# Kernel tuning notes

Measured on AMD Instinct MI355X. Metric: run time of the kernel, lower is better.

The kernel has to match this reference:

```python
import math
import jax, jax.numpy as jnp
import numpy as np

D_MODEL = 1024
L_MAX = 4096
BATCH = 2
FILTER_ORDER = 64
EMB_DIM = 3


def _make_z(L, emb_dim=EMB_DIM):
    # PositionalEmbedding: [time, real bands, imag bands] -> [1, L, emb_dim]
    t = jnp.linspace(0.0, 1.0, L)[None, :, None]
    bands = (emb_dim - 1) // 2
    t_res = jnp.linspace(0.0, L - 1.0, L)[None, :, None]
    w = 2.0 * math.pi * t_res / L
    f = jnp.linspace(1e-4, float(bands - 1), bands)[None, None]
    ph = f * w  # z = exp(-1j*ph) -> real=cos(ph), imag=-sin(ph)
    return jnp.concatenate([t, jnp.cos(ph), -jnp.sin(ph)], axis=-1).astype(jnp.float32)


def setup_inputs() -> dict:
    key = jax.random.key(0)
    ks = jax.random.split(key, 16)
    d = D_MODEL
    iw = 3 * d  # inner_width = d_model * (order + 1), order=2

    def rn(k, shape, scale):
        return (jax.random.normal(k, shape) * scale).astype(jnp.float32)

    return {
        'u': rn(ks[0], (BATCH, L_MAX, d), 1.0),
        'w_in': rn(ks[1], (iw, d), d ** -0.5),
        'b_in': rn(ks[2], (iw,), 0.01),
        'sf_w': rn(ks[3], (iw, 1, 3), 3 ** -0.5),
        'sf_b': rn(ks[4], (iw,), 0.01),
        'z': _make_z(L_MAX),
        'w0': rn(ks[5], (FILTER_ORDER, EMB_DIM), EMB_DIM ** -0.5),
        'b0': rn(ks[6], (FILTER_ORDER,), 0.01),
        'freq': jnp.ones((1, FILTER_ORDER), dtype=jnp.float32),  # Sin(w=1)
        'w1': rn(ks[7], (FILTER_ORDER, FILTER_ORDER), FILTER_ORDER ** -0.5),
        'b1': rn(ks[8], (FILTER_ORDER,), 0.01),
        'w2': rn(ks[9], (FILTER_ORDER, FILTER_ORDER), FILTER_ORDER ** -0.5),
        'b2': rn(ks[10], (FILTER_ORDER,), 0.01),
        'wf': rn(ks[11], (d, FILTER_ORDER), FILTER_ORDER ** -0.5),
        'D': rn(ks[12], (d,), 1.0),
        'w_out': rn(ks[13], (d, d), d ** -0.5),
        'b_out': rn(ks[14], (d,), 0.01),
    }


def _dwconv(x, w, b):
    # depthwise Conv1d(kernel=3, padding=2, groups=C); x: [B, C, L] -> [B, C, L+2]
    y = jax.lax.conv_general_dilated(
        x, w, window_strides=(1,), padding=[(2, 2)],
        feature_group_count=x.shape[1],
        dimension_numbers=('NCH', 'OIH', 'NCH'))
    return y + b[None, :, None]


def _fftconv(v, k, D):
    # circular conv via zero-padded FFT; torch's k_f/fft_size with norm='forward'
    # irfft cancels to the standard (norm='backward') inverse.
    L = v.shape[-1]
    n = 2 * L
    y = jnp.fft.irfft(jnp.fft.rfft(v, n=n) * jnp.fft.rfft(k, n=n), n=n)[..., :L]
    return y + v * D[:, None]


def reference(u, w_in, b_in, sf_w, sf_b, z, w0, b0, freq, w1, b1, w2, b2, wf, D, w_out, b_out):
    b, l, d = u.shape
    L = min(l, L_MAX)

    # input projection + short depthwise filter
    up = jnp.einsum('bld,ed->ble', u, w_in) + b_in  # [b, l, 3d]
    up = up.transpose(0, 2, 1)                       # [b, 3d, l]
    uc = _dwconv(up, sf_w, sf_b)[..., :L]            # [b, 3d, L]
    x0, x1, v = jnp.split(uc, 3, axis=1)             # each [b, d, L]

    # implicit filter MLP with shared Sin activation
    h = jnp.sin(freq * (z @ w0.T + b0))              # [1, L, 64]
    h = jnp.sin(freq * (h @ w1.T + b1))
    h = jnp.sin(freq * (h @ w2.T + b2))
    h = h @ wf.T                                     # [1, L, d]

    # exponential modulation (buffers: t, deltas)
    t = jnp.linspace(0.0, 1.0, L)[None, :, None]
    max_decay = math.log(0.01) / 0.3
    min_decay = math.log(0.01) / 1.5
    deltas = jnp.linspace(min_decay, max_decay, d)[None, None]
    h = h * jnp.exp(-t * jnp.abs(deltas))            # [1, L, d]
    k = h[0].T                                       # [d, L]

    # hyena recurrence (order=2 -> one gated fft conv)
    v = _fftconv(v * x1, k, D)
    y = (v * x0).transpose(0, 2, 1)                  # [b, L, d]
    return jnp.einsum('bld,ed->ble', y, w_out) + b_out
```

## Files before the change

kernel.cpp:

```cpp
#include <hip/hip_runtime.h>
#include <math.h>

#define DM   1024
#define LL   4096
#define NB   2
#define E3   3072
#define FPI  3.14159265358979323846f

typedef __bf16 bf16x8 __attribute__((ext_vector_type(8)));
typedef float  f32x4  __attribute__((ext_vector_type(4)));
typedef _Float16 f16x2 __attribute__((ext_vector_type(2)));

__device__ __forceinline__ unsigned short f2bf(float x) {
    unsigned u = __float_as_uint(x);
    u += 0x7fffu + ((u >> 16) & 1u);
    return (unsigned short)(u >> 16);
}
__device__ __forceinline__ void gload16(void* lds, const void* g) {
    typedef const __attribute__((address_space(1))) unsigned int* gp_t;
    typedef __attribute__((address_space(3))) unsigned int* lp_t;
    __builtin_amdgcn_global_load_lds((gp_t)g, (lp_t)lds, 16, 0, 0);
}

__global__ __launch_bounds__(256) void k_cvt_bf16(
    const float* __restrict__ in, ushort* __restrict__ out, int n4)
{
    int idx = blockIdx.x * 256 + threadIdx.x;
    int stride = gridDim.x * 256;
    for (int i = idx; i < n4; i += stride) {
        float4 v = reinterpret_cast<const float4*>(in)[i];
        ushort4 o;
        o.x = f2bf(v.x); o.y = f2bf(v.y); o.z = f2bf(v.z); o.w = f2bf(v.w);
        *reinterpret_cast<ushort4*>(out + 4 * i) = o;
    }
}

__global__ __launch_bounds__(512, 2) void k_gemm256(
    const ushort* __restrict__ A, const ushort* __restrict__ B,
    const float* __restrict__ bias, float* __restrict__ C,
    int Ntiles, int ldc)
{
    __shared__ __align__(16) char ldsm[131072];
    const int tid  = threadIdx.x;
    const int lane = tid & 63;
    const int w    = tid >> 6;
    const int wr   = w >> 2, wc = w & 3;

    const int cpx = gridDim.x >> 3;
    int swz = (blockIdx.x & 7) * cpx + (blockIdx.x >> 3);
    const int m0 = (swz / Ntiles) << 8;
    const int n0 = (swz % Ntiles) << 8;

    const int r0 = tid >> 2;
    const int swzc = ((tid & 3) ^ ((r0 >> 1) & 3)) << 4;
    const char* Asrc = (const char*)A + ((size_t)(m0 + r0) << 11) + swzc;
    const char* Bsrc = (const char*)B + ((size_t)(n0 + r0) << 11) + swzc;
    char* Ld = ldsm + tid * 16;

    const int lm = lane & 15, lk = lane >> 4;
    const int rA = wr * 128 + lm;
    const int rB = wc * 64 + lm;
    const int aBase = rA * 64 + ((lk ^ ((rA >> 1) & 3)) << 4);
    const int bBase = 32768 + rB * 64 + ((lk ^ ((rB >> 1) & 3)) << 4);

#define STG_A(ks, nb, t1) do { \
    gload16(Ld + (nb) + (ks)*16384,        Asrc + (t1)*128 + (ks)*64); \
    gload16(Ld + (nb) + (ks)*16384 + 8192, Asrc + (t1)*128 + (ks)*64 + 262144); } while(0)
#define STG_B(ks, nb, t1) do { \
    gload16(Ld + (nb) + 32768 + (ks)*16384,        Bsrc + (t1)*128 + (ks)*64); \
    gload16(Ld + (nb) + 32768 + (ks)*16384 + 8192, Bsrc + (t1)*128 + (ks)*64 + 262144); } while(0)
#define LDA(buf, ks, m) (*(const bf16x8*)(ldsm + (buf) + (ks)*16384 + aBase + (m)*1024))
#define LDB(buf, ks, n) (*(const bf16x8*)(ldsm + (buf) + (ks)*16384 + bBase + (n)*1024))
#define VMCNT4() asm volatile("s_waitcnt vmcnt(4)" ::: "memory")
#define VMCNT0() asm volatile("s_waitcnt vmcnt(0)" ::: "memory")
#define BAR() __builtin_amdgcn_s_barrier()

    f32x4 acc[8][4];
#pragma unroll
    for (int i = 0; i < 8; ++i)
#pragma unroll
        for (int j = 0; j < 4; ++j)
#pragma unroll
            for (int r = 0; r < 4; ++r) acc[i][j][r] = 0.f;

    STG_A(0, 0, 0); STG_B(0, 0, 0); STG_A(1, 0, 0); STG_B(1, 0, 0);
    VMCNT4();
    BAR();

    bf16x8 af[4], bq[4];
#pragma unroll 1
    for (int t = 0; t < 15; ++t) {
        const int buf = (t & 1) << 16;
        const int nb  = ((t + 1) & 1) << 16;
        const int t1  = t + 1;
#pragma unroll
        for (int n = 0; n < 4; ++n) bq[n] = LDB(buf, 0, n);
#pragma unroll
        for (int m = 0; m < 4; ++m) af[m] = LDA(buf, 0, m);
        STG_A(0, nb, t1);
        BAR();
        __builtin_amdgcn_s_setprio(1);
#pragma unroll
        for (int m = 0; m < 4; ++m)
#pragma unroll
            for (int n = 0; n < 4; ++n)
                acc[m][n] = __builtin_amdgcn_mfma_f32_16x16x32_bf16(af[m], bq[n], acc[m][n], 0, 0, 0);
        __builtin_amdgcn_s_setprio(0);
        BAR();
#pragma unroll
        for (int m = 0; m < 4; ++m) af[m] = LDA(buf, 0, 4 + m);
        STG_B(0, nb, t1);
        VMCNT4();
        BAR();
        __builtin_amdgcn_s_setprio(1);
#pragma unroll
        for (int m = 0; m < 4; ++m)
#pragma unroll
            for (int n = 0; n < 4; ++n)
                acc[4 + m][n] = __builtin_amdgcn_mfma_f32_16x16x32_bf16(af[m], bq[n], acc[4 + m][n], 0, 0, 0);
        __builtin_amdgcn_s_setprio(0);
        BAR();
#pragma unroll
        for (int n = 0; n < 4; ++n) bq[n] = LDB(buf, 1, n);
#pragma unroll
        for (int m = 0; m < 4; ++m) af[m] = LDA(buf, 1, m);
        STG_A(1, nb, t1);
        BAR();
        __builtin_amdgcn_s_setprio(1);
#pragma unroll
        for (int m = 0; m < 4; ++m)
#pragma unroll
            for (int n = 0; n < 4; ++n)
                acc[m][n] = __builtin_amdgcn_mfma_f32_16x16x32_bf16(af[m], bq[n], acc[m][n], 0, 0, 0);
        __builtin_amdgcn_s_setprio(0);
        BAR();
#pragma unroll
        for (int m = 0; m < 4; ++m) af[m] = LDA(buf, 1, 4 + m);
        STG_B(1, nb, t1);
        VMCNT4();
        BAR();
        __builtin_amdgcn_s_setprio(1);
#pragma unroll
        for (int m = 0; m < 4; ++m)
#pragma unroll
            for (int n = 0; n < 4; ++n)
                acc[4 + m][n] = __builtin_amdgcn_mfma_f32_16x16x32_bf16(af[m], bq[n], acc[4 + m][n], 0, 0, 0);
        __builtin_amdgcn_s_setprio(0);
        BAR();
    }
    {
        const int buf = 1 << 16;
#pragma unroll
        for (int n = 0; n < 4; ++n) bq[n] = LDB(buf, 0, n);
#pragma unroll
        for (int m = 0; m < 4; ++m) af[m] = LDA(buf, 0, m);
        BAR();
#pragma unroll
        for (int m = 0; m < 4; ++m)
#pragma unroll
            for (int n = 0; n < 4; ++n)
                acc[m][n] = __builtin_amdgcn_mfma_f32_16x16x32_bf16(af[m], bq[n], acc[m][n], 0, 0, 0);
        BAR();
#pragma unroll
        for (int m = 0; m < 4; ++m) af[m] = LDA(buf, 0, 4 + m);
        VMCNT0();
        BAR();
#pragma unroll
        for (int m = 0; m < 4; ++m)
#pragma unroll
            for (int n = 0; n < 4; ++n)
                acc[4 + m][n] = __builtin_amdgcn_mfma_f32_16x16x32_bf16(af[m], bq[n], acc[4 + m][n], 0, 0, 0);
        BAR();
#pragma unroll
        for (int n = 0; n < 4; ++n) bq[n] = LDB(buf, 1, n);
#pragma unroll
        for (int m = 0; m < 4; ++m) af[m] = LDA(buf, 1, m);
        BAR();
#pragma unroll
        for (int m = 0; m < 4; ++m)
#pragma unroll
            for (int n = 0; n < 4; ++n)
                acc[m][n] = __builtin_amdgcn_mfma_f32_16x16x32_bf16(af[m], bq[n], acc[m][n], 0, 0, 0);
        BAR();
#pragma unroll
        for (int m = 0; m < 4; ++m) af[m] = LDA(buf, 1, 4 + m);
        BAR();
#pragma unroll
        for (int m = 0; m < 4; ++m)
#pragma unroll
            for (int n = 0; n < 4; ++n)
                acc[4 + m][n] = __builtin_amdgcn_mfma_f32_16x16x32_bf16(af[m], bq[n], acc[4 + m][n], 0, 0, 0);
    }
    const int er = lk << 2, ec = lm;
#pragma unroll
    for (int m = 0; m < 8; ++m) {
        int row = m0 + wr * 128 + m * 16 + er;
#pragma unroll
        for (int n = 0; n < 4; ++n) {
            int col = n0 + wc * 64 + n * 16 + ec;
            float bz = bias[col];
            float* cp = C + (size_t)row * ldc + col;
#pragma unroll
            for (int r = 0; r < 4; ++r)
                cp[(size_t)r * ldc] = acc[m][n][r] + bz;
        }
    }
#undef STG_A
#undef STG_B
#undef LDA
#undef LDB
#undef VMCNT4
#undef VMCNT0
#undef BAR
}

__global__ __launch_bounds__(256) void k_gemm_bf16(
    const ushort* __restrict__ A, const ushort* __restrict__ B,
    const float* __restrict__ bias, float* __restrict__ C, int ldc)
{
    __shared__ ushort As[128 * 32];
    __shared__ ushort Bs[128 * 32];
    const int tid  = threadIdx.x;
    const int lane = tid & 63;
    const int w    = tid >> 6;
    const int wm   = (w >> 1) << 6, wn = (w & 1) << 6;
    const int m0   = blockIdx.y << 7, n0 = blockIdx.x << 7;

    f32x4 acc[4][4];
#pragma unroll
    for (int i = 0; i < 4; ++i)
#pragma unroll
        for (int j = 0; j < 4; ++j)
#pragma unroll
            for (int r = 0; r < 4; ++r) acc[i][j][r] = 0.f;

    const char* Ab = (const char*)A + ((size_t)(m0 + (tid >> 2)) << 11) + ((tid & 3) << 4);
    const char* Bb = (const char*)B + ((size_t)(n0 + (tid >> 2)) << 11) + ((tid & 3) << 4);
    char* AsD = (char*)As + tid * 16;
    char* BsD = (char*)Bs + tid * 16;
    const char* ap = (const char*)As + ((wm + (lane & 15)) << 6) + ((lane >> 4) << 4);
    const char* bp = (const char*)Bs + ((wn + (lane & 15)) << 6) + ((lane >> 4) << 4);

    for (int k0 = 0; k0 < 1024; k0 += 32) {
        __syncthreads();
        gload16(AsD,        Ab + k0 * 2);
        gload16(AsD + 4096, Ab + 131072 + k0 * 2);
        gload16(BsD,        Bb + k0 * 2);
        gload16(BsD + 4096, Bb + 131072 + k0 * 2);
        __syncthreads();
        bf16x8 af[4], bfr[4];
#pragma unroll
        for (int i = 0; i < 4; ++i) {
            af[i]  = *(const bf16x8*)(ap + (i << 10));
            bfr[i] = *(const bf16x8*)(bp + (i << 10));
        }
#pragma unroll
        for (int i = 0; i < 4; ++i)
#pragma unroll
            for (int j = 0; j < 4; ++j)
                acc[i][j] = __builtin_amdgcn_mfma_f32_16x16x32_bf16(
                    af[i], bfr[j], acc[i][j], 0, 0, 0);
    }
    const int er = (lane >> 4) << 2;
    const int ec = lane & 15;
#pragma unroll
    for (int i = 0; i < 4; ++i) {
        int row = m0 + wm + (i << 4) + er;
#pragma unroll
        for (int j = 0; j < 4; ++j) {
            int col = n0 + wn + (j << 4) + ec;
            float bz = bias[col];
            float* cp = C + (size_t)row * ldc + col;
#pragma unroll
            for (int r = 0; r < 4; ++r)
                cp[(size_t)r * ldc] = acc[i][j][r] + bz;
        }
    }
}

__global__ __launch_bounds__(256) void k_dwconv(
    const float* __restrict__ up, const float* __restrict__ sfw,
    const float* __restrict__ sfb, float* __restrict__ x0t,
    float* __restrict__ vin)
{
    __shared__ float xT[32][65];
    __shared__ float vT[32][65];
    const int b  = blockIdx.z;
    const int t0 = blockIdx.y * 64;
    const int c0 = blockIdx.x * 32;
    const int tid = threadIdx.x;
    const int cL = tid & 31, tL = tid >> 5;
    const float* upb = up + (size_t)b * LL * E3;
    const int c = c0 + cL;

#pragma unroll
    for (int r = 0; r < 8; ++r) {
        int t_local = (r << 3) + tL;
        int t = t0 + t_local;
        float res[3];
#pragma unroll
        for (int s3 = 0; s3 < 3; ++s3) {
            int e = c + (s3 << 10);
            float w0 = sfw[e*3+0], w1 = sfw[e*3+1], w2 = sfw[e*3+2];
            float xa = (t >= 2) ? upb[(size_t)(t-2)*E3 + e] : 0.f;
            float xb = (t >= 1) ? upb[(size_t)(t-1)*E3 + e] : 0.f;
            float xc = upb[(size_t)t*E3 + e];
            res[s3] = w0*xa + w1*xb + w2*xc + sfb[e];
        }
        xT[cL][t_local] = res[0];
        vT[cL][t_local] = res[1] * res[2];
    }
    __syncthreads();
    const int cW = tid >> 3, q = tid & 7;
    float tmp[8];
#pragma unroll
    for (int i = 0; i < 8; ++i) tmp[i] = xT[cW][8*q + i];
    size_t off = ((size_t)b * DM + c0 + cW) * LL + t0 + 8*q;
    *reinterpret_cast<float4*>(x0t + off)     = make_float4(tmp[0], tmp[1], tmp[2], tmp[3]);
    *reinterpret_cast<float4*>(x0t + off + 4) = make_float4(tmp[4], tmp[5], tmp[6], tmp[7]);
#pragma unroll
    for (int i = 0; i < 8; ++i) tmp[i] = vT[cW][8*q + i];
    *reinterpret_cast<float4*>(vin + off)     = make_float4(tmp[0], tmp[1], tmp[2], tmp[3]);
    *reinterpret_cast<float4*>(vin + off + 4) = make_float4(tmp[4], tmp[5], tmp[6], tmp[7]);
}

__global__ __launch_bounds__(256) void k_filt_mlp(
    const float* __restrict__ z, const float* __restrict__ w0,
    const float* __restrict__ b0, const float* __restrict__ fr,
    const float* __restrict__ w1, const float* __restrict__ b1,
    const float* __restrict__ w2, const float* __restrict__ b2,
    float* __restrict__ H3)
{
    __shared__ float w1t[64 * 65];
    __shared__ float w2t[64 * 65];
    __shared__ float hb[4][64];
    const int tid = threadIdx.x;
    for (int idx = tid; idx < 4096; idx += 256) {
        int j = idx >> 6, m = idx & 63;
        w1t[m*65 + j] = w1[idx];
        w2t[m*65 + j] = w2[idx];
    }
    __syncthreads();
    const int tl = tid >> 6, j = tid & 63;
    const float frj = fr[j];
    const float b0j = b0[j], b1j = b1[j], b2j = b2[j];
    const float w00 = w0[j*3+0], w01 = w0[j*3+1], w02 = w0[j*3+2];
    const int t0 = blockIdx.x * 64;
    for (int r = 0; r < 16; ++r) {
        int t = t0 + r*4 + tl;
        float z0 = z[t*3+0], z1 = z[t*3+1], z2 = z[t*3+2];
        float h = sinf(frj * (b0j + z0*w00 + z1*w01 + z2*w02));
        hb[tl][j] = h;
        __syncthreads();
        float s = b1j;
#pragma unroll
        for (int m = 0; m < 64; ++m) s = fmaf(hb[tl][m], w1t[m*65 + j], s);
        __syncthreads();
        h = sinf(frj * s);
        hb[tl][j] = h;
        __syncthreads();
        s = b2j;
#pragma unroll
        for (int m = 0; m < 64; ++m) s = fmaf(hb[tl][m], w2t[m*65 + j], s);
        h = sinf(frj * s);
        H3[(size_t)t * 64 + j] = h;
        __syncthreads();
    }
}

__global__ __launch_bounds__(256) void k_filt_k(
    const float* __restrict__ H3, const float* __restrict__ wf,
    float* __restrict__ kf)
{
    __shared__ float Hs[64][65];
    __shared__ float Ws[64][65];
    const int tid = threadIdx.x;
    const int t0 = blockIdx.x * 64, d0 = blockIdx.y * 64;
    for (int idx = tid; idx < 4096; idx += 256) {
        int r = idx >> 6, cc = idx & 63;
        Hs[r][cc] = H3[(size_t)(t0 + r) * 64 + cc];
        Ws[r][cc] = wf[(size_t)(d0 + r) * 64 + cc];
    }
    __syncthreads();
    const int tx = tid & 15, ty = tid >> 4;
    float acc[4][4];
#pragma unroll
    for (int i = 0; i < 4; ++i)
#pragma unroll
        for (int jj = 0; jj < 4; ++jj) acc[i][jj] = 0.f;
#pragma unroll
    for (int j = 0; j < 64; ++j) {
        float wv[4], hv[4];
#pragma unroll
        for (int i = 0; i < 4; ++i) wv[i] = Ws[4*ty + i][j];
#pragma unroll
        for (int i = 0; i < 4; ++i) hv[i] = Hs[4*tx + i][j];
#pragma unroll
        for (int i = 0; i < 4; ++i)
#pragma unroll
            for (int jj = 0; jj < 4; ++jj) acc[i][jj] = fmaf(wv[i], hv[jj], acc[i][jj]);
    }
    const float mind = -3.0701134573253944f;
    const float maxd = -15.350567286626972f;
#pragma unroll
    for (int i = 0; i < 4; ++i) {
        int d = d0 + 4*ty + i;
        float delta = fabsf(mind + (maxd - mind) * ((float)d / 1023.f));
#pragma unroll
        for (int jj = 0; jj < 4; ++jj) {
            int t = t0 + 4*tx + jj;
            float tn = (float)t / 4095.f;
            kf[(size_t)d * LL + t] = acc[i][jj] * expf(-tn * delta);
        }
    }
}

__device__ __forceinline__ int pidx(int p) { return p + (p >> 4); }

__device__ __forceinline__ float2 cmul(float2 a, float2 b) {
    return make_float2(a.x*b.x - a.y*b.y, a.x*b.y + a.y*b.x);
}

__device__ void fft_lds_fwd4(float2* buf, int tid) {
    int lh = 10;
#pragma unroll
    for (int h = 2048; h >= 32; h >>= 2, lh -= 2) {
        const int hh = h >> 1;
        const float rinv = -FPI / (float)h;
        __syncthreads();
#pragma unroll
        for (int r = 0; r < 4; ++r) {
            int bf = (r << 9) + tid;
            int q  = bf & (hh - 1);
            int g  = bf >> lh;
            int j  = (g << (lh + 2)) + q;
            float2 a = buf[pidx(j)];
            float2 b = buf[pidx(j + hh)];
            float2 c = buf[pidx(j + h)];
            float2 d = buf[pidx(j + h + hh)];
            float2 t0 = make_float2(a.x + c.x, a.y + c.y);
            float2 t1 = make_float2(a.x - c.x, a.y - c.y);
            float2 t2 = make_float2(b.x + d.x, b.y + d.y);
            float2 t3 = make_float2(b.y - d.y, d.x - b.x);
            float sn, cs;
            __sincosf(rinv * (float)q, &sn, &cs);
            float c2 = cs*cs - sn*sn, s2 = 2.f*cs*sn;
            float c3 = cs*c2 - sn*s2, s3 = cs*s2 + sn*c2;
            buf[pidx(j)] = make_float2(t0.x + t2.x, t0.y + t2.y);
            float2 e1 = make_float2(t0.x - t2.x, t0.y - t2.y);
            buf[pidx(j + hh)] = make_float2(e1.x*c2 - e1.y*s2, e1.x*s2 + e1.y*c2);
            float2 e2 = make_float2(t1.x + t3.x, t1.y + t3.y);
            buf[pidx(j + h)] = make_float2(e2.x*cs - e2.y*sn, e2.x*sn + e2.y*cs);
            float2 e3 = make_float2(t1.x - t3.x, t1.y - t3.y);
            buf[pidx(j + h + hh)] = make_float2(e3.x*c3 - e3.y*s3, e3.x*s3 + e3.y*c3);
        }
    }
    __syncthreads();
}

__device__ void fft_lds_inv4(float2* buf, int tid) {
    int lh = 4;
#pragma unroll
    for (int h = 32; h <= 2048; h <<= 2, lh += 2) {
        const int hh = h >> 1;
        const float rpos = FPI / (float)h;
        __syncthreads();
#pragma unroll
        for (int r = 0; r < 4; ++r) {
            int bf = (r << 9) + tid;
            int q  = bf & (hh - 1);
            int g  = bf >> lh;
            int j  = (g << (lh + 2)) + q;
            float2 o0 = buf[pidx(j)];
            float2 o1 = buf[pidx(j + hh)];
            float2 o2 = buf[pidx(j + h)];
            float2 o3 = buf[pidx(j + h + hh)];
            float sn, cs;
            __sincosf(rpos * (float)q, &sn, &cs);
            float c2 = cs*cs - sn*sn, s2 = 2.f*cs*sn;
            float c3 = cs*c2 - sn*s2, s3 = cs*s2 + sn*c2;
            float2 p1 = make_float2(o1.x*c2 - o1.y*s2, o1.x*s2 + o1.y*c2);
            float2 p2 = make_float2(o2.x*cs - o2.y*sn, o2.x*sn + o2.y*cs);
            float2 p3 = make_float2(o3.x*c3 - o3.y*s3, o3.x*s3 + o3.y*c3);
            float2 u0 = make_float2(o0.x + p1.x, o0.y + p1.y);
            float2 u1 = make_float2(o0.x - p1.x, o0.y - p1.y);
            float2 u2 = make_float2(p2.x + p3.x, p2.y + p3.y);
            float2 u3 = make_float2(p2.x - p3.x, p2.y - p3.y);
            float2 ib = make_float2(-u3.y, u3.x);
            buf[pidx(j)]          = make_float2(u0.x + u2.x, u0.y + u2.y);
            buf[pidx(j + hh)]     = make_float2(u1.x + ib.x, u1.y + ib.y);
            buf[pidx(j + h)]      = make_float2(u0.x - u2.x, u0.y - u2.y);
            buf[pidx(j + h + hh)] = make_float2(u1.x - ib.x, u1.y - ib.y);
        }
    }
    __syncthreads();
}

__device__ __forceinline__ void fft_reg_fwd(float2* c) {
    const float W16r[8] = {1.f, 0.92387953f, 0.70710678f, 0.38268343f,
                           0.f, -0.38268343f, -0.70710678f, -0.92387953f};
    const float W16i[8] = {0.f, -0.38268343f, -0.70710678f, -0.92387953f,
                           -1.f, -0.92387953f, -0.70710678f, -0.38268343f};
#pragma unroll
    for (int k = 0; k < 8; ++k) {
        float2 a = c[k], b = c[k+8];
        float2 d = make_float2(a.x - b.x, a.y - b.y);
        c[k]   = make_float2(a.x + b.x, a.y + b.y);
        c[k+8] = cmul(d, make_float2(W16r[k], W16i[k]));
    }
    const float W8r[4] = {1.f, 0.70710678f, 0.f, -0.70710678f};
    const float W8i[4] = {0.f, -0.70710678f, -1.f, -0.70710678f};
#pragma unroll
    for (int blk = 0; blk < 16; blk += 8)
#pragma unroll
        for (int k = 0; k < 4; ++k) {
            float2 a = c[blk+k], b = c[blk+k+4];
            float2 d = make_float2(a.x - b.x, a.y - b.y);
            c[blk+k]   = make_float2(a.x + b.x, a.y + b.y);
            c[blk+k+4] = cmul(d, make_float2(W8r[k], W8i[k]));
        }
#pragma unroll
    for (int blk = 0; blk < 16; blk += 4) {
        {   float2 a = c[blk], b = c[blk+2];
            c[blk]   = make_float2(a.x + b.x, a.y + b.y);
            c[blk+2] = make_float2(a.x - b.x, a.y - b.y); }
        {   float2 a = c[blk+1], b = c[blk+3];
            float2 d = make_float2(a.x - b.x, a.y - b.y);
            c[blk+1] = make_float2(a.x + b.x, a.y + b.y);
            c[blk+3] = make_float2(d.y, -d.x); }
    }
#pragma unroll
    for (int blk = 0; blk < 16; blk += 2) {
        float2 a = c[blk], b = c[blk+1];
        c[blk]   = make_float2(a.x + b.x, a.y + b.y);
        c[blk+1] = make_float2(a.x - b.x, a.y - b.y);
    }
}

__device__ __forceinline__ void fft_reg_inv(float2* c) {
#pragma unroll
    for (int blk = 0; blk < 16; blk += 2) {
        float2 a = c[blk], b = c[blk+1];
        c[blk]   = make_float2(a.x + b.x, a.y + b.y);
        c[blk+1] = make_float2(a.x - b.x, a.y - b.y);
    }
#pragma unroll
    for (int blk = 0; blk < 16; blk += 4) {
        {   float2 a = c[blk], b = c[blk+2];
            c[blk]   = make_float2(a.x + b.x, a.y + b.y);
            c[blk+2] = make_float2(a.x - b.x, a.y - b.y); }
        {   float2 a = c[blk+1], b = c[blk+3];
            float2 bt = make_float2(-c[blk+3].y, c[blk+3].x);
            c[blk+1] = make_float2(a.x + bt.x, a.y + bt.y);
            c[blk+3] = make_float2(a.x - bt.x, a.y - bt.y); }
    }
    const float W8r[4] = {1.f, 0.70710678f, 0.f, -0.70710678f};
    const float W8i[4] = {0.f, 0.70710678f, 1.f, 0.70710678f};
#pragma unroll
    for (int blk = 0; blk < 16; blk += 8)
#pragma unroll
        for (int k = 0; k < 4; ++k) {
            float2 a = c[blk+k], b = c[blk+k+4];
            float2 bt = cmul(b, make_float2(W8r[k], W8i[k]));
            c[blk+k]   = make_float2(a.x + bt.x, a.y + bt.y);
            c[blk+k+4] = make_float2(a.x - bt.x, a.y - bt.y);
        }
    const float W16r[8] = {1.f, 0.92387953f, 0.70710678f, 0.38268343f,
                           0.f, -0.38268343f, -0.70710678f, -0.92387953f};
    const float W16i[8] = {0.f, 0.38268343f, 0.70710678f, 0.92387953f,
                           1.f, 0.92387953f, 0.70710678f, 0.38268343f};
#pragma unroll
    for (int k = 0; k < 8; ++k) {
        float2 a = c[k], b = c[k+8];
        float2 bt = cmul(b, make_float2(W16r[k], W16i[k]));
        c[k]   = make_float2(a.x + bt.x, a.y + bt.y);
        c[k+8] = make_float2(a.x - bt.x, a.y - bt.y);
    }
}

__global__ __launch_bounds__(512) void k_kfft(
    const float* __restrict__ kf, f16x2* __restrict__ Kf)
{
    __shared__ float2 buf[8704];
    const int d = blockIdx.x, tid = threadIdx.x;
    const float* krow = kf + (size_t)d * LL;
    const float rinv0 = -FPI / 4096.f;
    for (int i = tid; i < 1024; i += 512) {
        float4 k4 = reinterpret_cast<const float4*>(krow)[i];
        int p = 4 * i;
        float kv[4] = {k4.x, k4.y, k4.z, k4.w};
#pragma unroll
        for (int q = 0; q < 4; ++q) {
            float sn, cs;
            __sincosf(rinv0 * (float)(p + q), &sn, &cs);
            buf[pidx(p + q)]        = make_float2(kv[q], 0.f);
            buf[pidx(p + q + 4096)] = make_float2(kv[q] * cs, kv[q] * sn);
        }
    }
    fft_lds_fwd4(buf, tid);
    float2 c[16];
    const int p0 = tid * 16;
#pragma unroll
    for (int j = 0; j < 16; ++j) c[j] = buf[pidx(p0 + j)];
    fft_reg_fwd(c);
    f16x2* outp = Kf + (size_t)d * 8192 + p0;
#pragma unroll
    for (int j = 0; j < 16; ++j) {
        f16x2 o;
        o[0] = (_Float16)(c[j].x * (1.f/8192.f));
        o[1] = (_Float16)(c[j].y * (1.f/8192.f));
        outp[j] = o;
    }
}

__global__ __launch_bounds__(512) void k_fftconv(
    const float* __restrict__ vin, const f16x2* __restrict__ Kf,
    const float* __restrict__ x0t, const float* __restrict__ Dp,
    ushort* __restrict__ yg)
{
    __shared__ float2 buf[8704];
    const int d = blockIdx.x, tid = threadIdx.x;
    const float* vrow0 = vin + (size_t)d * LL;
    const float* vrow1 = vin + ((size_t)DM + d) * LL;
    const float rinv0 = -FPI / 4096.f;
    for (int i = tid; i < 1024; i += 512) {
        float4 a4 = reinterpret_cast<const float4*>(vrow0)[i];
        float4 b4 = reinterpret_cast<const float4*>(vrow1)[i];
        int p = 4 * i;
        float ar[4] = {a4.x, a4.y, a4.z, a4.w};
        float br[4] = {b4.x, b4.y, b4.z, b4.w};
#pragma unroll
        for (int q = 0; q < 4; ++q) {
            float sn, cs;
            __sincosf(rinv0 * (float)(p + q), &sn, &cs);
            float2 z = make_float2(ar[q], br[q]);
            buf[pidx(p + q)]        = z;
            buf[pidx(p + q + 4096)] = cmul(z, make_float2(cs, sn));
        }
    }
    fft_lds_fwd4(buf, tid);
    float2 c[16];
    const int p0 = tid * 16;
#pragma unroll
    for (int j = 0; j < 16; ++j) c[j] = buf[pidx(p0 + j)];
    fft_reg_fwd(c);
    const f16x2* kfr = Kf + (size_t)d * 8192 + p0;
#pragma unroll
    for (int j = 0; j < 16; ++j) {
        f16x2 kv = kfr[j];
        c[j] = cmul(c[j], make_float2((float)kv[0], (float)kv[1]));
    }
    fft_reg_inv(c);
#pragma unroll
    for (int j = 0; j < 16; ++j) buf[pidx(p0 + j)] = c[j];
    fft_lds_inv4(buf, tid);
    const float Dd = Dp[d];
    const float* xrow0 = x0t + (size_t)d * LL;
    const float* xrow1 = x0t + ((size_t)DM + d) * LL;
    ushort* orow0 = yg + (size_t)d * LL;
    ushort* orow1 = yg + ((size_t)DM + d) * LL;
    const float rinv4 = FPI / 4096.f;
    for (int i = tid; i < 1024; i += 512) {
        float4 v0 = reinterpret_cast<const float4*>(vrow0)[i];
        float4 v1 = reinterpret_cast<const float4*>(vrow1)[i];
        float4 x0 = reinterpret_cast<const float4*>(xrow0)[i];
        float4 x1 = reinterpret_cast<const float4*>(xrow1)[i];
        int p = 4 * i;
        float vr0[4] = {v0.x, v0.y, v0.z, v0.w};
        float vr1[4] = {v1.x, v1.y, v1.z, v1.w};
        float xr0[4] = {x0.x, x0.y, x0.z, x0.w};
        float xr1[4] = {x1.x, x1.y, x1.z, x1.w};
        ushort s0[4], s1[4];
#pragma unroll
        for (int q = 0; q < 4; ++q) {
            float sn, cs;
            __sincosf(rinv4 * (float)(p + q), &sn, &cs);
            float2 a  = buf[pidx(p + q)];
            float2 bb = buf[pidx(p + q + 4096)];
            float2 bt = cmul(bb, make_float2(cs, sn));
            float yre = a.x + bt.x;
            float yim = a.y + bt.y;
            s0[q] = f2bf((yre + Dd * vr0[q]) * xr0[q]);
            s1[q] = f2bf((yim + Dd * vr1[q]) * xr1[q]);
        }
        *reinterpret_cast<ushort4*>(orow0 + p) = make_ushort4(s0[0], s0[1], s0[2], s0[3]);
        *reinterpret_cast<ushort4*>(orow1 + p) = make_ushort4(s1[0], s1[1], s1[2], s1[3]);
    }
}

__global__ __launch_bounds__(256) void k_tr(
    const ushort* __restrict__ yg, ushort* __restrict__ Ag)
{
    __shared__ ushort S[64][72];
    const int b  = blockIdx.z;
    const int d0 = blockIdx.y * 64;
    const int t0 = blockIdx.x * 64;
    const int tid = threadIdx.x;
#pragma unroll
    for (int p = 0; p < 2; ++p) {
        int idx = p * 256 + tid;
        int dr = idx >> 3, c8 = (idx & 7) << 3;
        uint4 v = *reinterpret_cast<const uint4*>(
            yg + ((size_t)b * DM + d0 + dr) * LL + t0 + c8);
        *reinterpret_cast<uint4*>(&S[dr][c8]) = v;
    }
    __syncthreads();
#pragma unroll
    for (int p = 0; p < 2; ++p) {
        int idx = p * 256 + tid;
        int tr = idx >> 3, dq = (idx & 7) << 3;
        ushort tmp[8] __attribute__((aligned(16)));
#pragma unroll
        for (int q = 0; q < 8; ++q) tmp[q] = S[dq + q][tr];
        *reinterpret_cast<uint4*>(Ag + ((size_t)b * LL + t0 + tr) * DM + d0 + dq) =
            *reinterpret_cast<uint4*>(tmp);
    }
}

extern "C" void kernel_launch(void* const* d_in, const int* in_sizes, int n_in,
                              void* d_out, int out_size, void* d_ws, size_t ws_size,
                              hipStream_t stream)
{
    if (n_in < 17) return;
    const float* u    = (const float*)d_in[0];
    const float* w_in = (const float*)d_in[1];
    const float* b_in = (const float*)d_in[2];
    const float* sf_w = (const float*)d_in[3];
    const float* sf_b = (const float*)d_in[4];
    const float* z    = (const float*)d_in[5];
    const float* w0   = (const float*)d_in[6];
    const float* b0   = (const float*)d_in[7];
    const float* freq = (const float*)d_in[8];
    const float* w1   = (const float*)d_in[9];
    const float* b1   = (const float*)d_in[10];
    const float* w2   = (const float*)d_in[11];
    const float* b2   = (const float*)d_in[12];
    const float* wf   = (const float*)d_in[13];
    const float* Dp   = (const float*)d_in[14];
    const float* wout = (const float*)d_in[15];
    const float* bout = (const float*)d_in[16];
    float* out = (float*)d_out;
    float* ws  = (float*)d_ws;

    float*  up    = ws;
    f16x2*  Kf    = (f16x2*)ws;
    float*  kfbuf = ws + 16777216;
    ushort* yg    = (ushort*)(ws + 16777216);
    float*  H3    = ws + 20971520;
    ushort* Ag    = (ushort*)(ws + 20971520);
    ushort* ub    = (ushort*)(ws + 25165824);
    float*  x0t   = ws + 25165824;
    ushort* wb    = (ushort*)(ws + 33554432);
    float*  vin   = ws + 33554432;
    ushort* woutb = (ushort*)(ws + 33554432);
    const size_t NEED = (size_t)41943040 * 4;
    if (ws_size < NEED) return;

    hipLaunchKernelGGL(k_cvt_bf16, dim3(2048), dim3(256), 0, stream, u, ub, 2097152);
    hipLaunchKernelGGL(k_cvt_bf16, dim3(2048), dim3(256), 0, stream, w_in, wb, 786432);
    hipLaunchKernelGGL(k_gemm256, dim3((8192/256) * (E3/256)), dim3(512), 0, stream,
                       ub, wb, b_in, up, E3/256, E3);
    hipLaunchKernelGGL(k_dwconv,   dim3(DM/32, LL/64, NB), dim3(256), 0, stream,
                       up, sf_w, sf_b, x0t, vin);
    hipLaunchKernelGGL(k_filt_mlp, dim3(LL/64), dim3(256), 0, stream,
                       z, w0, b0, freq, w1, b1, w2, b2, H3);
    hipLaunchKernelGGL(k_filt_k,   dim3(LL/64, DM/64), dim3(256), 0, stream,
                       H3, wf, kfbuf);
    hipLaunchKernelGGL(k_kfft,     dim3(DM), dim3(512), 0, stream,
                       kfbuf, Kf);
    hipLaunchKernelGGL(k_fftconv,  dim3(DM), dim3(512), 0, stream,
                       vin, Kf, x0t, Dp, yg);
    hipLaunchKernelGGL(k_cvt_bf16, dim3(1024), dim3(256), 0, stream, wout, woutb, 262144);
    hipLaunchKernelGGL(k_tr,       dim3(LL/64, DM/64, NB), dim3(256), 0, stream,
                       yg, Ag);
    hipLaunchKernelGGL(k_gemm_bf16, dim3(DM/128, 8192/128), dim3(256), 0, stream,
                       Ag, woutb, bout, out, DM);
}
```

Measured before the change: 267.5 us.

## Use 128x256 pipelined GEMM for both projections and store bf16 intermediate

The 256x256 input-projection GEMM becomes a 128x256 tile kernel with smaller LDS and more blocks. The same kernel now also replaces the simple output GEMM. The input projection writes bf16 instead of fp32 to halve that intermediate's traffic, and the depthwise conv reads bf16. The two fp32-to-bf16 conversions are merged into one launch. Rounding the projection output to bf16 lowers precision before the conv and gating.

```diff
diff --git a/kernel.cpp b/kernel.cpp
--- a/kernel.cpp
+++ b/kernel.cpp
@@ -16,10 +16,31 @@
     u += 0x7fffu + ((u >> 16) & 1u);
     return (unsigned short)(u >> 16);
 }
+__device__ __forceinline__ float bf2f(ushort s) {
+    return __uint_as_float(((unsigned)s) << 16);
+}
 __device__ __forceinline__ void gload16(void* lds, const void* g) {
     typedef const __attribute__((address_space(1))) unsigned int* gp_t;
     typedef __attribute__((address_space(3))) unsigned int* lp_t;
     __builtin_amdgcn_global_load_lds((gp_t)g, (lp_t)lds, 16, 0, 0);
+}
+
+__global__ __launch_bounds__(256) void k_cvt2(
+    const float* __restrict__ a, ushort* __restrict__ oa, int n4a,
+    const float* __restrict__ b, ushort* __restrict__ ob, int n4b)
+{
+    int idx = blockIdx.x * 256 + threadIdx.x;
+    int stride = gridDim.x * 256;
+    int tot = n4a + n4b;
+    for (int i = idx; i < tot; i += stride) {
+        const float4* src; ushort* dst; int k;
+        if (i < n4a) { src = (const float4*)a; dst = oa; k = i; }
+        else         { src = (const float4*)b; dst = ob; k = i - n4a; }
+        float4 v = src[k];
+        ushort4 o;
+        o.x = f2bf(v.x); o.y = f2bf(v.y); o.z = f2bf(v.z); o.w = f2bf(v.w);
+        *reinterpret_cast<ushort4*>(dst + 4 * k) = o;
+    }
 }
 
 __global__ __launch_bounds__(256) void k_cvt_bf16(
@@ -35,12 +56,12 @@
     }
 }
 
-__global__ __launch_bounds__(512, 2) void k_gemm256(
+__global__ __launch_bounds__(512, 1) void k_gemm128n(
     const ushort* __restrict__ A, const ushort* __restrict__ B,
-    const float* __restrict__ bias, float* __restrict__ C,
-    int Ntiles, int ldc)
-{
-    __shared__ __align__(16) char ldsm[131072];
+    const float* __restrict__ bias, void* __restrict__ Cv,
+    int Ntiles, int ldc, int obf)
+{
+    __shared__ __align__(16) char ldsm[98304];
     const int tid  = threadIdx.x;
     const int lane = tid & 63;
     const int w    = tid >> 6;
@@ -48,7 +69,7 @@
 
     const int cpx = gridDim.x >> 3;
     int swz = (blockIdx.x & 7) * cpx + (blockIdx.x >> 3);
-    const int m0 = (swz / Ntiles) << 8;
+    const int m0 = (swz / Ntiles) << 7;
     const int n0 = (swz % Ntiles) << 8;
 
     const int r0 = tid >> 2;
@@ -58,228 +79,156 @@
     char* Ld = ldsm + tid * 16;
 
     const int lm = lane & 15, lk = lane >> 4;
-    const int rA = wr * 128 + lm;
+    const int rA = wr * 64 + lm;
     const int rB = wc * 64 + lm;
     const int aBase = rA * 64 + ((lk ^ ((rA >> 1) & 3)) << 4);
-    const int bBase = 32768 + rB * 64 + ((lk ^ ((rB >> 1) & 3)) << 4);
-
-#define STG_A(ks, nb, t1) do { \
-    gload16(Ld + (nb) + (ks)*16384,        Asrc + (t1)*128 + (ks)*64); \
-    gload16(Ld + (nb) + (ks)*16384 + 8192, Asrc + (t1)*128 + (ks)*64 + 262144); } while(0)
+    const int bBase = 16384 + rB * 64 + ((lk ^ ((rB >> 1) & 3)) << 4);
+
+#define STG_A(ks, nb, t1) \
+    gload16(Ld + (nb) + (ks)*8192, Asrc + (t1)*128 + (ks)*64)
 #define STG_B(ks, nb, t1) do { \
-    gload16(Ld + (nb) + 32768 + (ks)*16384,        Bsrc + (t1)*128 + (ks)*64); \
-    gload16(Ld + (nb) + 32768 + (ks)*16384 + 8192, Bsrc + (t1)*128 + (ks)*64 + 262144); } while(0)
-#define LDA(buf, ks, m) (*(const bf16x8*)(ldsm + (buf) + (ks)*16384 + aBase + (m)*1024))
+    gload16(Ld + (nb) + 16384 + (ks)*16384,        Bsrc + (t1)*128 + (ks)*64); \
+    gload16(Ld + (nb) + 16384 + (ks)*16384 + 8192, Bsrc + (t1)*128 + (ks)*64 + 262144); } while(0)
+#define LDA(buf, ks, m) (*(const bf16x8*)(ldsm + (buf) + (ks)*8192 + aBase + (m)*1024))
 #define LDB(buf, ks, n) (*(const bf16x8*)(ldsm + (buf) + (ks)*16384 + bBase + (n)*1024))
-#define VMCNT4() asm volatile("s_waitcnt vmcnt(4)" ::: "memory")
+#define VMCNT3() asm volatile("s_waitcnt vmcnt(3)" ::: "memory")
 #define VMCNT0() asm volatile("s_waitcnt vmcnt(0)" ::: "memory")
 #define BAR() __builtin_amdgcn_s_barrier()
 
-    f32x4 acc[8][4];
-#pragma unroll
-    for (int i = 0; i < 8; ++i)
+    f32x4 acc[4][4];
+#pragma unroll
+    for (int i = 0; i < 4; ++i)
 #pragma unroll
         for (int j = 0; j < 4; ++j)
 #pragma unroll
             for (int r = 0; r < 4; ++r) acc[i][j][r] = 0.f;
 
     STG_A(0, 0, 0); STG_B(0, 0, 0); STG_A(1, 0, 0); STG_B(1, 0, 0);
-    VMCNT4();
+    VMCNT3();
     BAR();
 
-    bf16x8 af[4], bq[4];
+    bf16x8 af[2], bq[4];
 #pragma unroll 1
     for (int t = 0; t < 15; ++t) {
-        const int buf = (t & 1) << 16;
-        const int nb  = ((t + 1) & 1) << 16;
+        const int buf = (t & 1) * 49152;
+        const int nb  = 49152 - buf;
         const int t1  = t + 1;
 #pragma unroll
         for (int n = 0; n < 4; ++n) bq[n] = LDB(buf, 0, n);
-#pragma unroll
-        for (int m = 0; m < 4; ++m) af[m] = LDA(buf, 0, m);
+        af[0] = LDA(buf, 0, 0); af[1] = LDA(buf, 0, 1);
         STG_A(0, nb, t1);
         BAR();
         __builtin_amdgcn_s_setprio(1);
 #pragma unroll
-        for (int m = 0; m < 4; ++m)
+        for (int m = 0; m < 2; ++m)
 #pragma unroll
             for (int n = 0; n < 4; ++n)
                 acc[m][n] = __builtin_amdgcn_mfma_f32_16x16x32_bf16(af[m], bq[n], acc[m][n], 0, 0, 0);
         __builtin_amdgcn_s_setprio(0);
         BAR();
-#pragma unroll
-        for (int m = 0; m < 4; ++m) af[m] = LDA(buf, 0, 4 + m);
+        af[0] = LDA(buf, 0, 2); af[1] = LDA(buf, 0, 3);
         STG_B(0, nb, t1);
-        VMCNT4();
+        VMCNT3();
         BAR();
         __builtin_amdgcn_s_setprio(1);
 #pragma unroll
-        for (int m = 0; m < 4; ++m)
+        for (int m = 0; m < 2; ++m)
 #pragma unroll
             for (int n = 0; n < 4; ++n)
-                acc[4 + m][n] = __builtin_amdgcn_mfma_f32_16x16x32_bf16(af[m], bq[n], acc[4 + m][n], 0, 0, 0);
+                acc[2 + m][n] = __builtin_amdgcn_mfma_f32_16x16x32_bf16(af[m], bq[n], acc[2 + m][n], 0, 0, 0);
         __builtin_amdgcn_s_setprio(0);
         BAR();
 #pragma unroll
         for (int n = 0; n < 4; ++n) bq[n] = LDB(buf, 1, n);
-#pragma unroll
-        for (int m = 0; m < 4; ++m) af[m] = LDA(buf, 1, m);
+        af[0] = LDA(buf, 1, 0); af[1] = LDA(buf, 1, 1);
         STG_A(1, nb, t1);
         BAR();
         __builtin_amdgcn_s_setprio(1);
 #pragma unroll
-        for (int m = 0; m < 4; ++m)
+        for (int m = 0; m < 2; ++m)
 #pragma unroll
             for (int n = 0; n < 4; ++n)
                 acc[m][n] = __builtin_amdgcn_mfma_f32_16x16x32_bf16(af[m], bq[n], acc[m][n], 0, 0, 0);
         __builtin_amdgcn_s_setprio(0);
         BAR();
-#pragma unroll
-        for (int m = 0; m < 4; ++m) af[m] = LDA(buf, 1, 4 + m);
+        af[0] = LDA(buf, 1, 2); af[1] = LDA(buf, 1, 3);
         STG_B(1, nb, t1);
-        VMCNT4();
+        VMCNT3();
         BAR();
         __builtin_amdgcn_s_setprio(1);
 #pragma unroll
-        for (int m = 0; m < 4; ++m)
+        for (int m = 0; m < 2; ++m)
 #pragma unroll
             for (int n = 0; n < 4; ++n)
-                acc[4 + m][n] = __builtin_amdgcn_mfma_f32_16x16x32_bf16(af[m], bq[n], acc[4 + m][n], 0, 0, 0);
+                acc[2 + m][n] = __builtin_amdgcn_mfma_f32_16x16x32_bf16(af[m], bq[n], acc[2 + m][n], 0, 0, 0);
         __builtin_amdgcn_s_setprio(0);
         BAR();
     }
     {
-        const int buf = 1 << 16;
+        const int buf = 49152;
 #pragma unroll
         for (int n = 0; n < 4; ++n) bq[n] = LDB(buf, 0, n);
-#pragma unroll
-        for (int m = 0; m < 4; ++m) af[m] = LDA(buf, 0, m);
-        BAR();
-#pragma unroll
-        for (int m = 0; m < 4; ++m)
+        af[0] = LDA(buf, 0, 0); af[1] = LDA(buf, 0, 1);
+#pragma unroll
+        for (int m = 0; m < 2; ++m)
 #pragma unroll
             for (int n = 0; n < 4; ++n)
                 acc[m][n] = __builtin_amdgcn_mfma_f32_16x16x32_bf16(af[m], bq[n], acc[m][n], 0, 0, 0);
-        BAR();
-#pragma unroll
-        for (int m = 0; m < 4; ++m) af[m] = LDA(buf, 0, 4 + m);
+        af[0] = LDA(buf, 0, 2); af[1] = LDA(buf, 0, 3);
+#pragma unroll
+        for (int m = 0; m < 2; ++m)
+#pragma unroll
+            for (int n = 0; n < 4; ++n)
+                acc[2 + m][n] = __builtin_amdgcn_mfma_f32_16x16x32_bf16(af[m], bq[n], acc[2 + m][n], 0, 0, 0);
         VMCNT0();
         BAR();
 #pragma unroll
-        for (int m = 0; m < 4; ++m)
-#pragma unroll
-            for (int n = 0; n < 4; ++n)
-                acc[4 + m][n] = __builtin_amdgcn_mfma_f32_16x16x32_bf16(af[m], bq[n], acc[4 + m][n], 0, 0, 0);
-        BAR();
-#pragma unroll
         for (int n = 0; n < 4; ++n) bq[n] = LDB(buf, 1, n);
-#pragma unroll
-        for (int m = 0; m < 4; ++m) af[m] = LDA(buf, 1, m);
-        BAR();
-#pragma unroll
-        for (int m = 0; m < 4; ++m)
+        af[0] = LDA(buf, 1, 0); af[1] = LDA(buf, 1, 1);
+#pragma unroll
+        for (int m = 0; m < 2; ++m)
 #pragma unroll
             for (int n = 0; n < 4; ++n)
                 acc[m][n] = __builtin_amdgcn_mfma_f32_16x16x32_bf16(af[m], bq[n], acc[m][n], 0, 0, 0);
-        BAR();
-#pragma unroll
-        for (int m = 0; m < 4; ++m) af[m] = LDA(buf, 1, 4 + m);
-        BAR();
-#pragma unroll
-        for (int m = 0; m < 4; ++m)
+        af[0] = LDA(buf, 1, 2); af[1] = LDA(buf, 1, 3);
+#pragma unroll
+        for (int m = 0; m < 2; ++m)
 #pragma unroll
             for (int n = 0; n < 4; ++n)
-                acc[4 + m][n] = __builtin_amdgcn_mfma_f32_16x16x32_bf16(af[m], bq[n], acc[4 + m][n], 0, 0, 0);
+                acc[2 + m][n] = __builtin_amdgcn_mfma_f32_16x16x32_bf16(af[m], bq[n], acc[2 + m][n], 0, 0, 0);
     }
     const int er = lk << 2, ec = lm;
 #pragma unroll
-    for (int m = 0; m < 8; ++m) {
-        int row = m0 + wr * 128 + m * 16 + er;
+    for (int m = 0; m < 4; ++m) {
+        int row = m0 + wr * 64 + m * 16 + er;
 #pragma unroll
         for (int n = 0; n < 4; ++n) {
             int col = n0 + wc * 64 + n * 16 + ec;
             float bz = bias[col];
-            float* cp = C + (size_t)row * ldc + col;
-#pragma unroll
-            for (int r = 0; r < 4; ++r)
-                cp[(size_t)r * ldc] = acc[m][n][r] + bz;
+            if (obf) {
+                ushort* cp = (ushort*)Cv + (size_t)row * ldc + col;
+#pragma unroll
+                for (int r = 0; r < 4; ++r)
+                    cp[(size_t)r * ldc] = f2bf(acc[m][n][r] + bz);
+            } else {
+                float* cp = (float*)Cv + (size_t)row * ldc + col;
+#pragma unroll
+                for (int r = 0; r < 4; ++r)
+                    cp[(size_t)r * ldc] = acc[m][n][r] + bz;
+            }
         }
     }
 #undef STG_A
 #undef STG_B
 #undef LDA
 #undef LDB
-#undef VMCNT4
+#undef VMCNT3
 #undef VMCNT0
 #undef BAR
 }
 
-__global__ __launch_bounds__(256) void k_gemm_bf16(
-    const ushort* __restrict__ A, const ushort* __restrict__ B,
-    const float* __restrict__ bias, float* __restrict__ C, int ldc)
-{
-    __shared__ ushort As[128 * 32];
-    __shared__ ushort Bs[128 * 32];
-    const int tid  = threadIdx.x;
-    const int lane = tid & 63;
-    const int w    = tid >> 6;
-    const int wm   = (w >> 1) << 6, wn = (w & 1) << 6;
-    const int m0   = blockIdx.y << 7, n0 = blockIdx.x << 7;
-
-    f32x4 acc[4][4];
-#pragma unroll
-    for (int i = 0; i < 4; ++i)
-#pragma unroll
-        for (int j = 0; j < 4; ++j)
-#pragma unroll
-            for (int r = 0; r < 4; ++r) acc[i][j][r] = 0.f;
-
-    const char* Ab = (const char*)A + ((size_t)(m0 + (tid >> 2)) << 11) + ((tid & 3) << 4);
-    const char* Bb = (const char*)B + ((size_t)(n0 + (tid >> 2)) << 11) + ((tid & 3) << 4);
-    char* AsD = (char*)As + tid * 16;
-    char* BsD = (char*)Bs + tid * 16;
-    const char* ap = (const char*)As + ((wm + (lane & 15)) << 6) + ((lane >> 4) << 4);
-    const char* bp = (const char*)Bs + ((wn + (lane & 15)) << 6) + ((lane >> 4) << 4);
-
-    for (int k0 = 0; k0 < 1024; k0 += 32) {
-        __syncthreads();
-        gload16(AsD,        Ab + k0 * 2);
-        gload16(AsD + 4096, Ab + 131072 + k0 * 2);
-        gload16(BsD,        Bb + k0 * 2);
-        gload16(BsD + 4096, Bb + 131072 + k0 * 2);
-        __syncthreads();
-        bf16x8 af[4], bfr[4];
-#pragma unroll
-        for (int i = 0; i < 4; ++i) {
-            af[i]  = *(const bf16x8*)(ap + (i << 10));
-            bfr[i] = *(const bf16x8*)(bp + (i << 10));
-        }
-#pragma unroll
-        for (int i = 0; i < 4; ++i)
-#pragma unroll
-            for (int j = 0; j < 4; ++j)
-                acc[i][j] = __builtin_amdgcn_mfma_f32_16x16x32_bf16(
-                    af[i], bfr[j], acc[i][j], 0, 0, 0);
-    }
-    const int er = (lane >> 4) << 2;
-    const int ec = lane & 15;
-#pragma unroll
-    for (int i = 0; i < 4; ++i) {
-        int row = m0 + wm + (i << 4) + er;
-#pragma unroll
-        for (int j = 0; j < 4; ++j) {
-            int col = n0 + wn + (j << 4) + ec;
-            float bz = bias[col];
-            float* cp = C + (size_t)row * ldc + col;
-#pragma unroll
-            for (int r = 0; r < 4; ++r)
-                cp[(size_t)r * ldc] = acc[i][j][r] + bz;
-        }
-    }
-}
-
 __global__ __launch_bounds__(256) void k_dwconv(
-    const float* __restrict__ up, const float* __restrict__ sfw,
+    const ushort* __restrict__ up, const float* __restrict__ sfw,
     const float* __restrict__ sfb, float* __restrict__ x0t,
     float* __restrict__ vin)
 {
@@ -290,7 +239,7 @@
     const int c0 = blockIdx.x * 32;
     const int tid = threadIdx.x;
     const int cL = tid & 31, tL = tid >> 5;
-    const float* upb = up + (size_t)b * LL * E3;
+    const ushort* upb = up + (size_t)b * LL * E3;
     const int c = c0 + cL;
 
 #pragma unroll
@@ -302,9 +251,9 @@
         for (int s3 = 0; s3 < 3; ++s3) {
             int e = c + (s3 << 10);
             float w0 = sfw[e*3+0], w1 = sfw[e*3+1], w2 = sfw[e*3+2];
-            float xa = (t >= 2) ? upb[(size_t)(t-2)*E3 + e] : 0.f;
-            float xb = (t >= 1) ? upb[(size_t)(t-1)*E3 + e] : 0.f;
-            float xc = upb[(size_t)t*E3 + e];
+            float xa = (t >= 2) ? bf2f(upb[(size_t)(t-2)*E3 + e]) : 0.f;
+            float xb = (t >= 1) ? bf2f(upb[(size_t)(t-1)*E3 + e]) : 0.f;
+            float xc = bf2f(upb[(size_t)t*E3 + e]);
             res[s3] = w0*xa + w1*xb + w2*xc + sfb[e];
         }
         xT[cL][t_local] = res[0];
@@ -742,7 +691,7 @@
     float* out = (float*)d_out;
     float* ws  = (float*)d_ws;
 
-    float*  up    = ws;
+    ushort* up    = (ushort*)ws;
     f16x2*  Kf    = (f16x2*)ws;
     float*  kfbuf = ws + 16777216;
     ushort* yg    = (ushort*)(ws + 16777216);
@@ -756,10 +705,10 @@
     const size_t NEED = (size_t)41943040 * 4;
     if (ws_size < NEED) return;
 
-    hipLaunchKernelGGL(k_cvt_bf16, dim3(2048), dim3(256), 0, stream, u, ub, 2097152);
-    hipLaunchKernelGGL(k_cvt_bf16, dim3(2048), dim3(256), 0, stream, w_in, wb, 786432);
-    hipLaunchKernelGGL(k_gemm256, dim3((8192/256) * (E3/256)), dim3(512), 0, stream,
-                       ub, wb, b_in, up, E3/256, E3);
+    hipLaunchKernelGGL(k_cvt2,     dim3(2048), dim3(256), 0, stream,
+                       u, ub, 2097152, w_in, wb, 786432);
+    hipLaunchKernelGGL(k_gemm128n, dim3((8192/128) * (E3/256)), dim3(512), 0, stream,
+                       ub, wb, b_in, (void*)up, E3/256, E3, 1);
     hipLaunchKernelGGL(k_dwconv,   dim3(DM/32, LL/64, NB), dim3(256), 0, stream,
                        up, sf_w, sf_b, x0t, vin);
     hipLaunchKernelGGL(k_filt_mlp, dim3(LL/64), dim3(256), 0, stream,
@@ -773,6 +722,6 @@
     hipLaunchKernelGGL(k_cvt_bf16, dim3(1024), dim3(256), 0, stream, wout, woutb, 262144);
     hipLaunchKernelGGL(k_tr,       dim3(LL/64, DM/64, NB), dim3(256), 0, stream,
                        yg, Ag);
-    hipLaunchKernelGGL(k_gemm_bf16, dim3(DM/128, 8192/128), dim3(256), 0, stream,
-                       Ag, woutb, bout, out, DM);
-}
+    hipLaunchKernelGGL(k_gemm128n, dim3((8192/128) * (DM/256)), dim3(512), 0, stream,
+                       Ag, woutb, bout, (void*)out, DM/256, DM, 0);
+}
```

New measurement: 283.5 us. +6.0%, slower.
